# Performance work log

Measured on AMD Instinct MI355X. Metric: run time of the kernel, lower is better.

## Reference

```python
import jax, jax.numpy as jnp
import numpy as np

BS, T, X_DIM = 16, 4096, 256


def setup_inputs() -> dict:
    key = jax.random.key(0)
    kx, kb, kl = jax.random.split(key, 3)
    x_set = jax.random.normal(kx, (BS, T, X_DIM), dtype=jnp.float32)
    # Match torch.nn.init.orthogonal_ via QR of a Gaussian matrix
    B, _ = jnp.linalg.qr(jax.random.normal(kb, (X_DIM, X_DIM), dtype=jnp.float32))
    Lam, _ = jnp.linalg.qr(jax.random.normal(kl, (X_DIM, X_DIM), dtype=jnp.float32))
    return {"x_set": x_set, "B": B.astype(jnp.float32), "Lam": Lam.astype(jnp.float32)}


def reference(x_set, B, Lam):
    # Original computes h_T = sum_{j=0}^{T} Lambda^j @ B @ x_{T-j} (O(T^2)).
    # Equivalent linear recurrence: h_t = Lambda @ h_{t-1} + B @ x_t, h_{-1} = 0.
    Bx = jnp.einsum('de,bte->btd', B, x_set)          # [bs, T, d]

    def step(h, bx_t):
        h = jnp.einsum('de,be->bd', Lam, h) + bx_t    # [bs, d]
        return h, h

    h0 = jnp.zeros((x_set.shape[0], x_set.shape[2]), dtype=x_set.dtype)
    _, hs = jax.lax.scan(step, h0, jnp.swapaxes(Bx, 0, 1))  # [T, bs, d]
    return jnp.swapaxes(hs, 0, 1)                            # [bs, T, d]
```

## Files before the change

kernel.cpp:

```cpp
#include <hip/hip_runtime.h>
#include <hip/hip_bf16.h>
#include <stdint.h>


#define CHUNK  64

typedef short v8s __attribute__((ext_vector_type(8)));
typedef float v4f __attribute__((ext_vector_type(4)));

static __device__ __forceinline__ unsigned short f2u(float f) {
  union { float f; unsigned int u; } x; x.f = f;
  unsigned int u = x.u + 0x7FFFu + ((x.u >> 16) & 1u);
  return (unsigned short)(u >> 16);
}
static __device__ __forceinline__ float u2f(unsigned short h) {
  union { unsigned int u; float f; } x; x.u = ((unsigned int)h) << 16;
  return x.f;
}
static __device__ __forceinline__ void lds_barrier() {
  asm volatile("s_waitcnt lgkmcnt(0)\n\ts_barrier" ::: "memory");
}

template<bool A_F32, bool C_BF16, bool ADD_C>
__global__ __launch_bounds__(256) void gemm_tile(
    const void* __restrict__ Ap, const unsigned short* __restrict__ Bp,
    void* __restrict__ Cp, int lda, int ldb, int ldc, int Kper, long csplit)
{
  __shared__ unsigned short As[64][72];
  __shared__ unsigned short Bst[64][72];
  const int tid = threadIdx.x;
  const int lane = tid & 63, w = tid >> 6;
  const int q = lane >> 4, ln = lane & 15;
  const long n0 = (long)blockIdx.x * 64;
  const long m0 = (long)blockIdx.y * 64;
  const int  kz = blockIdx.z;
  const long kbase = (long)kz * Kper;
  const int sm = tid >> 2;
  const int sk = (tid & 3) << 4;

  v4f acc[4];
#pragma unroll
  for (int i = 0; i < 4; ++i) acc[i] = 0;

  float4 fA[4];
  v8s aR0, aR1, bR0, bR1;

  auto load_tile = [&](long kg) {
    if (A_F32) {
      const float* A = (const float*)Ap + (m0 + sm) * (long)lda + kg + sk;
#pragma unroll
      for (int t = 0; t < 4; ++t) fA[t] = ((const float4*)A)[t];
    } else {
      const unsigned short* A = (const unsigned short*)Ap + (m0 + sm) * (long)lda + kg + sk;
      aR0 = ((const v8s*)A)[0]; aR1 = ((const v8s*)A)[1];
    }
    const unsigned short* Bg = Bp + (kg + sm) * (long)ldb + n0 + sk;
    bR0 = ((const v8s*)Bg)[0]; bR1 = ((const v8s*)Bg)[1];
  };

  load_tile(kbase);

  for (int ks = 0; ks < Kper; ks += 64) {
    __syncthreads();
    if (A_F32) {
      unsigned short* d = &As[sm][sk];
#pragma unroll
      for (int t = 0; t < 4; ++t) {
        d[4*t+0] = f2u(fA[t].x); d[4*t+1] = f2u(fA[t].y);
        d[4*t+2] = f2u(fA[t].z); d[4*t+3] = f2u(fA[t].w);
      }
    } else {
      *(v8s*)&As[sm][sk] = aR0; *(v8s*)&As[sm][sk + 8] = aR1;
    }
#pragma unroll
    for (int r = 0; r < 8; ++r) Bst[sk + r][sm] = (unsigned short)bR0[r];
#pragma unroll
    for (int r = 0; r < 8; ++r) Bst[sk + 8 + r][sm] = (unsigned short)bR1[r];
    __syncthreads();
    if (ks + 64 < Kper) load_tile(kbase + ks + 64);
#pragma unroll
    for (int kb = 0; kb < 64; kb += 32) {
      v8s a = *(const v8s*)&As[w*16 + ln][kb + q*8];
#pragma unroll
      for (int nb = 0; nb < 4; ++nb) {
        v8s b = *(const v8s*)&Bst[nb*16 + ln][kb + q*8];
        acc[nb] = __builtin_amdgcn_mfma_f32_16x16x32_bf16(a, b, acc[nb], 0, 0, 0);
      }
    }
  }
#pragma unroll
  for (int nb = 0; nb < 4; ++nb)
#pragma unroll
    for (int r = 0; r < 4; ++r) {
      const long row = m0 + w*16 + q*4 + r;
      const long col = n0 + nb*16 + ln;
      float v = acc[nb][r];
      if (C_BF16) ((unsigned short*)Cp)[row * (long)ldc + col] = f2u(v);
      else {
        float* Cf = (float*)Cp + (long)kz * csplit;
        if (ADD_C) v += Cf[row * (long)ldc + col];
        Cf[row * (long)ldc + col] = v;
      }
    }
}

__global__ __launch_bounds__(256) void pow_round(
    unsigned short* __restrict__ Phi, unsigned short* __restrict__ Plo, int mpow,
    unsigned short* __restrict__ Phi2, unsigned short* __restrict__ Plo2)
{
  __shared__ unsigned short As[64][72];
  __shared__ unsigned short Bst[64][72];
  const int tid = threadIdx.x, lane = tid & 63, w = tid >> 6;
  const int q = lane >> 4, ln = lane & 15;
  const int jj = (blockIdx.x >> 2) + 1;
  const int n0 = (blockIdx.x & 3) * 64;
  const int m0 = blockIdx.y * 64;
  const unsigned short* Ah = Phi + (size_t)mpow * 65536;
  const unsigned short* Al = Plo + (size_t)mpow * 65536;
  const unsigned short* Bh = Phi + (size_t)jj * 65536;
  const unsigned short* Bl = Plo + (size_t)jj * 65536;
  const int sm = tid >> 2, sk = (tid & 3) << 4;
  v4f acc[4];
#pragma unroll
  for (int i = 0; i < 4; ++i) acc[i] = 0;

  v8s aR0, aR1, bR0, bR1;
  auto load_tile = [&](int it) {
    const int seg = it >> 2, ks = (it & 3) << 6;
    const unsigned short* Asrc = (seg == 1) ? Al : Ah;
    const unsigned short* Bsrc = (seg == 2) ? Bl : Bh;
    const unsigned short* Ag = Asrc + (size_t)(m0 + sm) * 256 + ks + sk;
    aR0 = ((const v8s*)Ag)[0]; aR1 = ((const v8s*)Ag)[1];
    const unsigned short* Bg = Bsrc + (size_t)(ks + sm) * 256 + n0 + sk;
    bR0 = ((const v8s*)Bg)[0]; bR1 = ((const v8s*)Bg)[1];
  };

  load_tile(0);
  for (int it = 0; it < 12; ++it) {
    __syncthreads();
    *(v8s*)&As[sm][sk] = aR0; *(v8s*)&As[sm][sk + 8] = aR1;
#pragma unroll
    for (int r = 0; r < 8; ++r) Bst[sk + r][sm] = (unsigned short)bR0[r];
#pragma unroll
    for (int r = 0; r < 8; ++r) Bst[sk + 8 + r][sm] = (unsigned short)bR1[r];
    __syncthreads();
    if (it + 1 < 12) load_tile(it + 1);
#pragma unroll
    for (int kb = 0; kb < 64; kb += 32) {
      v8s a = *(const v8s*)&As[w*16 + ln][kb + q*8];
#pragma unroll
      for (int nb = 0; nb < 4; ++nb) {
        v8s bb = *(const v8s*)&Bst[nb*16 + ln][kb + q*8];
        acc[nb] = __builtin_amdgcn_mfma_f32_16x16x32_bf16(a, bb, acc[nb], 0, 0, 0);
      }
    }
  }
  const size_t ob = (size_t)(mpow + jj) * 65536;
#pragma unroll
  for (int nb = 0; nb < 4; ++nb)
#pragma unroll
    for (int r = 0; r < 4; ++r) {
      const int row = m0 + w*16 + q*4 + r;
      const int col = n0 + nb*16 + ln;
      float v = acc[nb][r];
      unsigned short hi = f2u(v);
      Phi[ob + (size_t)row*256 + col] = hi;
      Plo[ob + (size_t)row*256 + col] = f2u(v - u2f(hi));
      if (mpow == 32) {
        if (jj == 32) {
          Phi2[65536 + (size_t)row*256 + col] = hi;
          Plo2[65536 + (size_t)row*256 + col] = f2u(v - u2f(hi));
        } else if (jj == 1) {
          Phi2[(size_t)row*256 + col] = (row == col) ? (unsigned short)0x3F80 : (unsigned short)0;
          Plo2[(size_t)row*256 + col] = 0;
        }
      }
    }
}

__global__ __launch_bounds__(256) void pack_init(
    const float* __restrict__ Bm, const float* __restrict__ Lam,
    unsigned short* __restrict__ Bt, unsigned short* __restrict__ LamT,
    unsigned short* __restrict__ Phi, unsigned short* __restrict__ Plo)
{
  const int idx = blockIdx.x * 256 + threadIdx.x;
  const int e = idx >> 8, d = idx & 255;
  Bt[idx]   = f2u(Bm[d * 256 + e]);
  LamT[idx] = f2u(Lam[d * 256 + e]);
  float v = Lam[idx];
  unsigned short hi = f2u(v);
  Phi[65536 + idx] = hi;
  Plo[65536 + idx] = f2u(v - u2f(hi));
  const int dd = idx >> 8, ee = idx & 255;
  Phi[idx] = (dd == ee) ? (unsigned short)0x3F80 : (unsigned short)0;
  Plo[idx] = 0;
}

__global__ __launch_bounds__(256) void pack_all(
    const unsigned short* __restrict__ Phi,
    const unsigned short* __restrict__ Phi2, const unsigned short* __restrict__ Plo2,
    unsigned short* __restrict__ Ghat,
    unsigned short* __restrict__ Qcat, unsigned short* __restrict__ G2,
    unsigned short* __restrict__ LcT2hi, unsigned short* __restrict__ LcT2lo)
{
  __shared__ unsigned short tile[64][65];
  const int tx = threadIdx.x & 63, ty = threadIdx.x >> 6;
  const int blk0 = blockIdx.x;
  if (blk0 < 1024) {
    const int jpar = blk0 >> 4, t16 = blk0 & 15;
    const unsigned short* src = Phi + (size_t)(63 - jpar) * 65536;
    const int d0 = (t16 & 3) * 64, e0 = (t16 >> 2) * 64;
#pragma unroll
    for (int s = 0; s < 16; ++s)
      tile[ty*16 + s][tx] = src[(size_t)(d0 + ty*16 + s) * 256 + e0 + tx];
    __syncthreads();
#pragma unroll
    for (int s = 0; s < 16; ++s) {
      const int e = e0 + ty*16 + s, d = d0 + tx;
      Ghat[((size_t)(jpar*256 + e)) * 256 + d] = tile[tx][ty*16 + s];
    }
    return;
  }
  const int blk = blk0 - 1024;
  if (blk < 1152) {
    const int rt = blk >> 5, ct = blk & 31;
    const int k0 = rt * 64, c0 = ct * 64;
    const int r = c0 >> 8, d0 = c0 & 255;
    int p = 0, e0 = 0;
    bool zero = false;
    if (k0 < 256) { p = r; e0 = k0; }
    else {
      const int u = (k0 - 256) >> 8; e0 = (k0 - 256) & 255;
      if (u >= r) zero = true; else p = r - 1 - u;
    }
    if (zero) {
#pragma unroll
      for (int s = 0; s < 16; ++s)
        Qcat[(size_t)(k0 + ty*16 + s) * 2048 + c0 + tx] = 0;
      return;
    }
    const unsigned short* src = Phi2 + (size_t)p * 65536;
#pragma unroll
    for (int s = 0; s < 16; ++s)
      tile[ty*16 + s][tx] = src[(size_t)(d0 + ty*16 + s) * 256 + e0 + tx];
    __syncthreads();
#pragma unroll
    for (int s = 0; s < 16; ++s)
      Qcat[(size_t)(k0 + ty*16 + s) * 2048 + c0 + tx] = tile[tx][ty*16 + s];
  } else if (blk < 1280) {
    const int t = blk - 1152;
    const int rt = t >> 2, ct = t & 3;
    const int k0 = rt * 64, d0 = ct * 64;
    const int r = k0 >> 8, e0 = k0 & 255;
    const unsigned short* src = Phi2 + (size_t)(7 - r) * 65536;
#pragma unroll
    for (int s = 0; s < 16; ++s)
      tile[ty*16 + s][tx] = src[(size_t)(d0 + ty*16 + s) * 256 + e0 + tx];
    __syncthreads();
#pragma unroll
    for (int s = 0; s < 16; ++s)
      G2[(size_t)(k0 + ty*16 + s) * 256 + d0 + tx] = tile[tx][ty*16 + s];
  } else {
    const int t = blk - 1280;
    const int half = t >> 4, t16 = t & 15;
    const int d0 = (t16 & 3) * 64, e0 = (t16 >> 2) * 64;
    const unsigned short* src = (half ? Plo2 : Phi2) + (size_t)8 * 65536;
    unsigned short* dst = half ? LcT2lo : LcT2hi;
#pragma unroll
    for (int s = 0; s < 16; ++s)
      tile[ty*16 + s][tx] = src[(size_t)(d0 + ty*16 + s) * 256 + e0 + tx];
    __syncthreads();
#pragma unroll
    for (int s = 0; s < 16; ++s)
      dst[(size_t)(e0 + ty*16 + s) * 256 + d0 + tx] = tile[tx][ty*16 + s];
  }
}

__global__ __launch_bounds__(256) void reduce_s2(
    const float* __restrict__ Sp, unsigned short* __restrict__ Acat)
{
  const int f = blockIdx.x * 256 + threadIdx.x;
  float v = 0;
#pragma unroll
  for (int z = 0; z < 8; ++z) v += Sp[(size_t)z * 262144 + f];
  const int e = f & 255, i = (f >> 8) & 63, b = f >> 14;
  const int u = i & 7, m = i >> 3;
  Acat[(size_t)(b*8 + m) * 2304 + 256 + u*256 + e] = f2u(v);
}

__global__ __launch_bounds__(512, 2) void k4b_combine(
    const unsigned short* __restrict__ LcT2hi, const unsigned short* __restrict__ LcT2lo,
    const float* __restrict__ S2, unsigned short* __restrict__ Acat)
{
  __shared__ unsigned short Hhi[16][264];
  __shared__ unsigned short Hlo[16][264];
  const int tid = threadIdx.x, lane = tid & 63, w = tid >> 6;
  const int q = lane >> 4, ln = lane & 15;

  v8s bhi[8][2], blo[8][2];
#pragma unroll
  for (int kk = 0; kk < 8; ++kk)
#pragma unroll
    for (int nb = 0; nb < 2; ++nb) {
      const int n = 32*w + nb*16 + ln;
#pragma unroll
      for (int r = 0; r < 8; ++r) {
        const int k = kk*32 + q*8 + r;
        bhi[kk][nb][r] = (short)LcT2hi[k*256 + n];
        blo[kk][nb][r] = (short)LcT2lo[k*256 + n];
      }
    }
  for (int e = tid; e < 16*264; e += 512) { (&Hhi[0][0])[e] = 0; (&Hlo[0][0])[e] = 0; }
  lds_barrier();

  for (int m = 0; m < 8; ++m) {
    for (int e = tid; e < 4096; e += 512) {
      const int b = e >> 8, d = e & 255;
      Acat[(size_t)(b*8 + m) * 2304 + d] = Hhi[b][d];
    }
    v8s ahi[8], alo[8];
#pragma unroll
    for (int kk = 0; kk < 8; ++kk) {
      ahi[kk] = *(const v8s*)&Hhi[ln][kk*32 + q*8];
      alo[kk] = *(const v8s*)&Hlo[ln][kk*32 + q*8];
    }
    lds_barrier();
    v4f acc[2];
#pragma unroll
    for (int nb = 0; nb < 2; ++nb)
#pragma unroll
      for (int r = 0; r < 4; ++r) {
        const int bb = 4*q + r, col = 32*w + nb*16 + ln;
        acc[nb][r] = S2[(size_t)(bb*8 + m) * 256 + col];
      }
#pragma unroll
    for (int kk = 0; kk < 8; ++kk)
#pragma unroll
      for (int nb = 0; nb < 2; ++nb) {
        acc[nb] = __builtin_amdgcn_mfma_f32_16x16x32_bf16(ahi[kk], bhi[kk][nb], acc[nb], 0, 0, 0);
        acc[nb] = __builtin_amdgcn_mfma_f32_16x16x32_bf16(alo[kk], bhi[kk][nb], acc[nb], 0, 0, 0);
        acc[nb] = __builtin_amdgcn_mfma_f32_16x16x32_bf16(ahi[kk], blo[kk][nb], acc[nb], 0, 0, 0);
      }
#pragma unroll
    for (int nb = 0; nb < 2; ++nb)
#pragma unroll
      for (int r = 0; r < 4; ++r) {
        const int bb = 4*q + r, col = 32*w + nb*16 + ln;
        float v = acc[nb][r];
        unsigned short hi = f2u(v);
        Hhi[bb][col] = hi;
        Hlo[bb][col] = f2u(v - u2f(hi));
      }
    lds_barrier();
  }
}

__global__ __launch_bounds__(256, 1) void k5_scan(
    const unsigned short* __restrict__ LamT,
    const unsigned short* __restrict__ Bx,
    const unsigned short* __restrict__ Abf, float* __restrict__ Out)
{
  __shared__ unsigned short gs[2][16][264];
  const int tid = threadIdx.x, lane = tid & 63, w = tid >> 6;
  const int q = lane >> 4, ln = lane & 15;
  const int blk = blockIdx.x;
  const int b  = blk >> 4;
  const int i0 = (blk * 4) & 63;

  v8s bf[8][4];
#pragma unroll
  for (int kk = 0; kk < 8; ++kk)
#pragma unroll
    for (int nb = 0; nb < 4; ++nb) {
      const int n = 64*w + nb*16 + ln;
#pragma unroll
      for (int r = 0; r < 8; ++r)
        bf[kk][nb][r] = (short)LamT[(kk*32 + q*8 + r) * 256 + n];
    }
  for (int e = tid; e < 16*264; e += 256) (&gs[0][0][0])[e] = 0;
  lds_barrier();
#pragma unroll
  for (int r = 0; r < 4; ++r)
    gs[0][r][tid] = Abf[((size_t)(b*64 + i0 + r)) * 256 + tid];

  size_t base[4];
#pragma unroll
  for (int r = 0; r < 4; ++r)
    base[r] = ((size_t)b*4096 + (size_t)(i0 + r)*64) * 256;
  const int colw = 64*w;

  unsigned short bxr[2][4][4];
  if (q == 0) {
#pragma unroll
    for (int s = 0; s < 2; ++s)
#pragma unroll
      for (int r = 0; r < 4; ++r)
#pragma unroll
        for (int nb = 0; nb < 4; ++nb)
          bxr[s][r][nb] = Bx[base[r] + (size_t)s*256 + colw + nb*16 + ln];
  }
  lds_barrier();

#pragma unroll 2
  for (int j = 0; j < CHUNK; ++j) {
    v8s a[8];
#pragma unroll
    for (int kk = 0; kk < 8; ++kk) a[kk] = *(const v8s*)&gs[j & 1][ln][kk*32 + q*8];
    v4f acc[4];
#pragma unroll
    for (int nb = 0; nb < 4; ++nb) acc[nb] = 0;
#pragma unroll
    for (int kk = 0; kk < 8; ++kk)
#pragma unroll
      for (int nb = 0; nb < 4; ++nb)
        acc[nb] = __builtin_amdgcn_mfma_f32_16x16x32_bf16(a[kk], bf[kk][nb], acc[nb], 0, 0, 0);
    if (q == 0) {
#pragma unroll
      for (int r = 0; r < 4; ++r) {
        const size_t rb = base[r] + (size_t)j*256 + colw;
#pragma unroll
        for (int nb = 0; nb < 4; ++nb) {
          const float g = acc[nb][r] + u2f(bxr[j & 1][r][nb]);
          Out[rb + nb*16 + ln] = g;
          gs[(j + 1) & 1][r][colw + nb*16 + ln] = f2u(g);
        }
      }
      if (j < CHUNK - 2) {
#pragma unroll
        for (int r = 0; r < 4; ++r) {
          const size_t rb = base[r] + (size_t)(j + 2)*256 + colw;
#pragma unroll
          for (int nb = 0; nb < 4; ++nb)
            bxr[j & 1][r][nb] = Bx[rb + nb*16 + ln];
        }
      }
    }
    lds_barrier();
  }
}

extern "C" void kernel_launch(void* const* d_in, const int* in_sizes, int n_in,
                              void* d_out, int out_size, void* d_ws, size_t ws_size,
                              hipStream_t stream)
{
  const float* x   = (const float*)d_in[0];
  const float* Bm  = (const float*)d_in[1];
  const float* Lam = (const float*)d_in[2];
  float* Out = (float*)d_out;
  (void)in_sizes; (void)n_in; (void)out_size; (void)ws_size;

  char* ws = (char*)d_ws;
  size_t off = 0;
  auto alloc = [&](size_t bytes) { void* p = ws + off; off += (bytes + 255) & ~(size_t)255; return p; };
  unsigned short* Bx    = (unsigned short*)alloc((size_t)16777216 * 2);
  unsigned short* Phi   = (unsigned short*)alloc((size_t)65 * 65536 * 2);
  unsigned short* Plo   = (unsigned short*)alloc((size_t)65 * 65536 * 2);
  unsigned short* Ghat  = (unsigned short*)alloc((size_t)16384 * 256 * 2);
  unsigned short* Qcat  = (unsigned short*)alloc((size_t)2304 * 2048 * 2);
  unsigned short* G2    = (unsigned short*)alloc((size_t)2048 * 256 * 2);
  unsigned short* Phi2  = (unsigned short*)alloc((size_t)9 * 65536 * 2);
  unsigned short* Plo2  = (unsigned short*)alloc((size_t)9 * 65536 * 2);
  unsigned short* Bt    = (unsigned short*)alloc(131072);
  unsigned short* LamT  = (unsigned short*)alloc(131072);
  unsigned short* LcT2hi= (unsigned short*)alloc(131072);
  unsigned short* LcT2lo= (unsigned short*)alloc(131072);
  unsigned short* Acat  = (unsigned short*)alloc((size_t)128 * 2304 * 2);
  float*          S2    = (float*)alloc(131072);
  unsigned short* Abf   = (unsigned short*)alloc(524288);
  float*          Spart = (float*)Plo;

  pack_init<<<dim3(256), dim3(256), 0, stream>>>(Bm, Lam, Bt, LamT, Phi, Plo);
  gemm_tile<true, true, false><<<dim3(4, 1024, 1), dim3(256), 0, stream>>>(
      (const void*)x, Bt, (void*)Bx, 256, 256, 256, 256, 0);
  for (int mp = 1; mp <= 32; mp <<= 1)
    pow_round<<<dim3(mp * 4, 4, 1), dim3(256), 0, stream>>>(Phi, Plo, mp, Phi2, Plo2);
  for (int mp = 1; mp <= 4; mp <<= 1)
    pow_round<<<dim3(mp * 4, 4, 1), dim3(256), 0, stream>>>(Phi2, Plo2, mp, Phi2, Plo2);
  pack_all<<<dim3(2336), dim3(256), 0, stream>>>(Phi, Phi2, Plo2,
      Ghat, Qcat, G2, LcT2hi, LcT2lo);
  gemm_tile<false, false, false><<<dim3(4, 16, 8), dim3(256), 0, stream>>>(
      (const void*)Bx, Ghat, (void*)Spart, 16384, 256, 256, 2048, 262144);
  reduce_s2<<<dim3(1024), dim3(256), 0, stream>>>(Spart, Acat);
  gemm_tile<false, false, false><<<dim3(4, 2, 1), dim3(256), 0, stream>>>(
      (const void*)(Acat + 256), G2, (void*)S2, 2304, 256, 256, 2048, 0);
  k4b_combine<<<dim3(1), dim3(512), 0, stream>>>(LcT2hi, LcT2lo, S2, Acat);
  gemm_tile<false, true, false><<<dim3(32, 2, 1), dim3(256), 0, stream>>>(
      (const void*)Acat, Qcat, (void*)Abf, 2304, 2048, 2048, 2304, 0);
  k5_scan<<<dim3(256), dim3(256), 0, stream>>>(LamT, Bx, Abf, Out);
}
```

Measured before the change: 400.6 us.

## Widen pow_round to 512 threads and spread scan row outputs across quads

pow_round now runs 8 waves per block with a 128-wide K tile, half the iterations, and each wave computing a 16x32 output slice, so more waves share the small power-doubling GEMMs. In k5_scan, the four recurrent rows are placed at LDS rows 0,4,8,12 so each quad lane group owns one row's epilogue. Stores and Bx prefetches are thereby spread over all 64 lanes instead of only q==0. The aim is to cut the serial epilogue latency per scan step and the pow_round critical path, at the cost of larger LDS tiles and more MFMA padding rows.

```diff
diff --git a/kernel.cpp b/kernel.cpp
--- a/kernel.cpp
+++ b/kernel.cpp
@@ -104,64 +104,66 @@
     }
 }
 
-__global__ __launch_bounds__(256) void pow_round(
+__global__ __launch_bounds__(512) void pow_round(
     unsigned short* __restrict__ Phi, unsigned short* __restrict__ Plo, int mpow,
     unsigned short* __restrict__ Phi2, unsigned short* __restrict__ Plo2)
 {
-  __shared__ unsigned short As[64][72];
-  __shared__ unsigned short Bst[64][72];
+  __shared__ unsigned short As[64][136];
+  __shared__ unsigned short Bst[64][136];
   const int tid = threadIdx.x, lane = tid & 63, w = tid >> 6;
   const int q = lane >> 4, ln = lane & 15;
   const int jj = (blockIdx.x >> 2) + 1;
   const int n0 = (blockIdx.x & 3) * 64;
   const int m0 = blockIdx.y * 64;
+  const int mb = w >> 1, nh = w & 1;
   const unsigned short* Ah = Phi + (size_t)mpow * 65536;
   const unsigned short* Al = Plo + (size_t)mpow * 65536;
   const unsigned short* Bh = Phi + (size_t)jj * 65536;
   const unsigned short* Bl = Plo + (size_t)jj * 65536;
-  const int sm = tid >> 2, sk = (tid & 3) << 4;
-  v4f acc[4];
-#pragma unroll
-  for (int i = 0; i < 4; ++i) acc[i] = 0;
+  const int sm  = tid >> 3, sk  = (tid & 7) << 4;
+  const int smk = tid >> 2, snk = (tid & 3) << 4;
+  v4f acc[2];
+#pragma unroll
+  for (int i = 0; i < 2; ++i) acc[i] = 0;
 
   v8s aR0, aR1, bR0, bR1;
   auto load_tile = [&](int it) {
-    const int seg = it >> 2, ks = (it & 3) << 6;
+    const int seg = it >> 1, ks = (it & 1) << 7;
     const unsigned short* Asrc = (seg == 1) ? Al : Ah;
     const unsigned short* Bsrc = (seg == 2) ? Bl : Bh;
     const unsigned short* Ag = Asrc + (size_t)(m0 + sm) * 256 + ks + sk;
     aR0 = ((const v8s*)Ag)[0]; aR1 = ((const v8s*)Ag)[1];
-    const unsigned short* Bg = Bsrc + (size_t)(ks + sm) * 256 + n0 + sk;
+    const unsigned short* Bg = Bsrc + (size_t)(ks + smk) * 256 + n0 + snk;
     bR0 = ((const v8s*)Bg)[0]; bR1 = ((const v8s*)Bg)[1];
   };
 
   load_tile(0);
-  for (int it = 0; it < 12; ++it) {
+  for (int it = 0; it < 6; ++it) {
     __syncthreads();
     *(v8s*)&As[sm][sk] = aR0; *(v8s*)&As[sm][sk + 8] = aR1;
 #pragma unroll
-    for (int r = 0; r < 8; ++r) Bst[sk + r][sm] = (unsigned short)bR0[r];
-#pragma unroll
-    for (int r = 0; r < 8; ++r) Bst[sk + 8 + r][sm] = (unsigned short)bR1[r];
-    __syncthreads();
-    if (it + 1 < 12) load_tile(it + 1);
-#pragma unroll
-    for (int kb = 0; kb < 64; kb += 32) {
-      v8s a = *(const v8s*)&As[w*16 + ln][kb + q*8];
-#pragma unroll
-      for (int nb = 0; nb < 4; ++nb) {
-        v8s bb = *(const v8s*)&Bst[nb*16 + ln][kb + q*8];
+    for (int r = 0; r < 8; ++r) Bst[snk + r][smk] = (unsigned short)bR0[r];
+#pragma unroll
+    for (int r = 0; r < 8; ++r) Bst[snk + 8 + r][smk] = (unsigned short)bR1[r];
+    __syncthreads();
+    if (it + 1 < 6) load_tile(it + 1);
+#pragma unroll
+    for (int kb = 0; kb < 128; kb += 32) {
+      v8s a = *(const v8s*)&As[mb*16 + ln][kb + q*8];
+#pragma unroll
+      for (int nb = 0; nb < 2; ++nb) {
+        v8s bb = *(const v8s*)&Bst[nh*32 + nb*16 + ln][kb + q*8];
         acc[nb] = __builtin_amdgcn_mfma_f32_16x16x32_bf16(a, bb, acc[nb], 0, 0, 0);
       }
     }
   }
   const size_t ob = (size_t)(mpow + jj) * 65536;
 #pragma unroll
-  for (int nb = 0; nb < 4; ++nb)
+  for (int nb = 0; nb < 2; ++nb)
 #pragma unroll
     for (int r = 0; r < 4; ++r) {
-      const int row = m0 + w*16 + q*4 + r;
-      const int col = n0 + nb*16 + ln;
+      const int row = m0 + mb*16 + q*4 + r;
+      const int col = n0 + nh*32 + nb*16 + ln;
       float v = acc[nb][r];
       unsigned short hi = f2u(v);
       Phi[ob + (size_t)row*256 + col] = hi;
@@ -377,28 +379,21 @@
       for (int r = 0; r < 8; ++r)
         bf[kk][nb][r] = (short)LamT[(kk*32 + q*8 + r) * 256 + n];
     }
-  for (int e = tid; e < 16*264; e += 256) (&gs[0][0][0])[e] = 0;
+  for (int e = tid; e < 2*16*264; e += 256) (&gs[0][0][0])[e] = 0;
   lds_barrier();
 #pragma unroll
   for (int r = 0; r < 4; ++r)
-    gs[0][r][tid] = Abf[((size_t)(b*64 + i0 + r)) * 256 + tid];
-
-  size_t base[4];
-#pragma unroll
-  for (int r = 0; r < 4; ++r)
-    base[r] = ((size_t)b*4096 + (size_t)(i0 + r)*64) * 256;
+    gs[0][4*r][tid] = Abf[((size_t)(b*64 + i0 + r)) * 256 + tid];
+
+  const size_t baseq = ((size_t)b*4096 + (size_t)(i0 + q)*64) * 256;
   const int colw = 64*w;
 
-  unsigned short bxr[2][4][4];
-  if (q == 0) {
-#pragma unroll
-    for (int s = 0; s < 2; ++s)
-#pragma unroll
-      for (int r = 0; r < 4; ++r)
-#pragma unroll
-        for (int nb = 0; nb < 4; ++nb)
-          bxr[s][r][nb] = Bx[base[r] + (size_t)s*256 + colw + nb*16 + ln];
-  }
+  unsigned short bxr[2][4];
+#pragma unroll
+  for (int s = 0; s < 2; ++s)
+#pragma unroll
+    for (int nb = 0; nb < 4; ++nb)
+      bxr[s][nb] = Bx[baseq + (size_t)s*256 + colw + nb*16 + ln];
   lds_barrier();
 
 #pragma unroll 2
@@ -414,25 +409,19 @@
 #pragma unroll
       for (int nb = 0; nb < 4; ++nb)
         acc[nb] = __builtin_amdgcn_mfma_f32_16x16x32_bf16(a[kk], bf[kk][nb], acc[nb], 0, 0, 0);
-    if (q == 0) {
-#pragma unroll
-      for (int r = 0; r < 4; ++r) {
-        const size_t rb = base[r] + (size_t)j*256 + colw;
-#pragma unroll
-        for (int nb = 0; nb < 4; ++nb) {
-          const float g = acc[nb][r] + u2f(bxr[j & 1][r][nb]);
-          Out[rb + nb*16 + ln] = g;
-          gs[(j + 1) & 1][r][colw + nb*16 + ln] = f2u(g);
-        }
+    {
+      const size_t rb = baseq + (size_t)j*256 + colw;
+#pragma unroll
+      for (int nb = 0; nb < 4; ++nb) {
+        const float g = acc[nb][0] + u2f(bxr[j & 1][nb]);
+        Out[rb + nb*16 + ln] = g;
+        gs[(j + 1) & 1][4*q][colw + nb*16 + ln] = f2u(g);
       }
       if (j < CHUNK - 2) {
-#pragma unroll
-        for (int r = 0; r < 4; ++r) {
-          const size_t rb = base[r] + (size_t)(j + 2)*256 + colw;
-#pragma unroll
-          for (int nb = 0; nb < 4; ++nb)
-            bxr[j & 1][r][nb] = Bx[rb + nb*16 + ln];
-        }
+        const size_t rb2 = baseq + (size_t)(j + 2)*256 + colw;
+#pragma unroll
+        for (int nb = 0; nb < 4; ++nb)
+          bxr[j & 1][nb] = Bx[rb2 + nb*16 + ln];
       }
     }
     lds_barrier();
@@ -473,9 +462,9 @@
   gemm_tile<true, true, false><<<dim3(4, 1024, 1), dim3(256), 0, stream>>>(
       (const void*)x, Bt, (void*)Bx, 256, 256, 256, 256, 0);
   for (int mp = 1; mp <= 32; mp <<= 1)
-    pow_round<<<dim3(mp * 4, 4, 1), dim3(256), 0, stream>>>(Phi, Plo, mp, Phi2, Plo2);
+    pow_round<<<dim3(mp * 4, 4, 1), dim3(512), 0, stream>>>(Phi, Plo, mp, Phi2, Plo2);
   for (int mp = 1; mp <= 4; mp <<= 1)
-    pow_round<<<dim3(mp * 4, 4, 1), dim3(256), 0, stream>>>(Phi2, Plo2, mp, Phi2, Plo2);
+    pow_round<<<dim3(mp * 4, 4, 1), dim3(512), 0, stream>>>(Phi2, Plo2, mp, Phi2, Plo2);
   pack_all<<<dim3(2336), dim3(256), 0, stream>>>(Phi, Phi2, Plo2,
       Ghat, Qcat, G2, LcT2hi, LcT2lo);
   gemm_tile<false, false, false><<<dim3(4, 16, 8), dim3(256), 0, stream>>>(
```

After: 366.9 us. 1.09x faster.
